# Kernel optimization log

Hardware: AMD Instinct MI355X
Metric: run time of the kernel (lower is better)

Reference implementation:

```python
import jax, jax.numpy as jnp
import numpy as np

N_CELLS = 50000
HID = 64
DEG = 16
K_NODES = 4  # nodes per cell; cell i owns nodes [4i, 4i+4)
SP = 3


def setup_inputs() -> dict:
    key = jax.random.key(0)
    ks = jax.random.split(key, 12)
    s = 1.0 / np.sqrt(HID)
    inp = {
        'features': jax.random.normal(ks[0], (N_CELLS, HID), jnp.float32),
        'positions': jax.random.normal(ks[1], (K_NODES * N_CELLS, SP), jnp.float32),
        'neighbors': jax.random.randint(ks[2], (N_CELLS, DEG), 0, N_CELLS, jnp.int32),
        # message MLP: Linear(2H+1 -> H), SiLU, Linear(H -> H)
        'W1': jax.random.normal(ks[3], (2 * HID + 1, HID), jnp.float32) * s,
        'b1': jnp.zeros((HID,), jnp.float32),
        'W2': jax.random.normal(ks[4], (HID, HID), jnp.float32) * s,
        'b2': jnp.zeros((HID,), jnp.float32),
        # update MLP: Linear(H + H -> H), SiLU, Linear(H -> H)
        'Wu1': jax.random.normal(ks[5], (2 * HID, HID), jnp.float32) * s,
        'bu1': jnp.zeros((HID,), jnp.float32),
        'Wu2': jax.random.normal(ks[6], (HID, HID), jnp.float32) * s,
        'bu2': jnp.zeros((HID,), jnp.float32),
    }
    return inp


def reference(features, positions, neighbors, W1, b1, W2, b2, Wu1, bu1, Wu2, bu2):
    N, H = features.shape
    # centroid of each cell's owned nodes (cell i -> nodes [K*i, K*i+K))
    cent = positions.reshape(N, K_NODES, SP).mean(axis=1)          # [N, sp]
    fj = features[neighbors]                                       # [N, D, H]
    cj = cent[neighbors]                                           # [N, D, sp]
    # centroid-distance geometric invariant per (cell, neighbor) pair
    geom = jnp.linalg.norm(cent[:, None, :] - cj, axis=-1, keepdims=True)  # [N, D, 1]
    fi = jnp.broadcast_to(features[:, None, :], fj.shape)          # [N, D, H]
    x = jnp.concatenate([fi, fj, geom], axis=-1)                   # [N, D, 2H+1]
    h = jax.nn.silu(x @ W1 + b1) @ W2 + b2                         # [N, D, H]
    msg = h.mean(axis=1)                                           # mean over neighbors
    u = jnp.concatenate([features, msg], axis=-1)                  # [N, 2H]
    upd = jax.nn.silu(u @ Wu1 + bu1) @ Wu2 + bu2
    updated_features = features + upd
    return updated_features, positions
```

## Files before the change

kernel.cpp:

```cpp
#include <hip/hip_runtime.h>


#define DEG 16

typedef __attribute__((ext_vector_type(8))) short short8;
typedef __attribute__((ext_vector_type(4))) float f32x4;
typedef uint2 uint2_a __attribute__((may_alias));
typedef uint4 uint4_a __attribute__((may_alias));
typedef unsigned short ushort_a __attribute__((may_alias));

union HbRd { uint4_a u; short8 s; };
union Frag { short8 s; uint4 u; };

__device__ __forceinline__ unsigned f2bf(float f) {
  unsigned u = __float_as_uint(f);
  return (u + 0x7FFFu + ((u >> 16) & 1u)) >> 16;
}
__device__ __forceinline__ float bf2f(unsigned bits16) {
  return __uint_as_float(bits16 << 16);
}
__device__ __forceinline__ float silu(float h) {
  return h / (1.f + __expf(-h));
}
__device__ __forceinline__ float silu_fast(float h) {
  return h * __builtin_amdgcn_rcpf(1.f + __expf(-h));
}

__global__ __launch_bounds__(256) void aux_kernel(
    const float* __restrict__ pos,
    const float* __restrict__ W1, const float* __restrict__ W2,
    const float* __restrict__ Wu1, const float* __restrict__ Wu2,
    float* __restrict__ outpos, float* __restrict__ cent4,
    unsigned short* __restrict__ w1pq, unsigned short* __restrict__ w2t,
    unsigned short* __restrict__ wu1t, unsigned short* __restrict__ wu2b)
{
  int t = blockIdx.x * 256 + threadIdx.x;
  if (t < 150000) {
    ((float4*)outpos)[t] = ((const float4*)pos)[t];
  } else if (t < 174576) {
    const int r = t - 150000;
    if (r < 8192) {
      const int j = r & 7, l = (r >> 3) & 15, q = (r >> 7) & 3;
      const int f = r >> 9, kk = f & 1, mt = f >> 1;
      const int k = kk * 32 + q * 8 + j;
      const int m = mt * 16 + l;
      w1pq[r] = (unsigned short)f2bf(
          (m < 64) ? W1[k * 64 + m] : W1[(k + 64) * 64 + (m - 64)]);
    } else if (r < 12288) {
      const int s = r - 8192;
      const int j = s & 7, l = (s >> 3) & 15, q = (s >> 7) & 3;
      const int f = s >> 9, kk = f & 1, mt = f >> 1;
      const int k = kk * 32 + q * 8 + j;
      w2t[s] = (unsigned short)f2bf(W2[k * 64 + mt * 16 + l]);
    } else if (r < 20480) {
      const int s = r - 12288;
      const int j = s & 7, l = (s >> 3) & 15, q = (s >> 7) & 3;
      const int f = s >> 9, kk = f & 3, mt = f >> 2;
      const int k = kk * 32 + q * 8 + j;
      wu1t[s] = (unsigned short)f2bf(Wu1[k * 64 + mt * 16 + l]);
    } else {
      const int s = r - 20480;
      const int j = s & 7, l = (s >> 3) & 15, q = (s >> 7) & 3;
      const int f = s >> 9, kk = f & 1, nt = f >> 1;
      const int k = kk * 32 + q * 8 + j;
      wu2b[s] = (unsigned short)f2bf(Wu2[k * 64 + nt * 16 + l]);
    }
  } else if (t < 224576) {
    const int i = t - 174576;
    const float4* pp = (const float4*)(pos + 12 * i);
    const float4 a = pp[0], b = pp[1], c = pp[2];
    float4 o;
    o.x = (a.x + a.w + b.z + c.y) * 0.25f;
    o.y = (a.y + b.x + b.w + c.z) * 0.25f;
    o.z = (a.z + b.y + c.x + c.w) * 0.25f;
    o.w = 0.f;
    ((float4*)cent4)[i] = o;
  }
}

__global__ __launch_bounds__(256) void prep_kernel(
    const float* __restrict__ feat,
    const unsigned short* __restrict__ w1pq,
    unsigned short* __restrict__ featb,
    unsigned char* __restrict__ Q8)
{
  const int lane = threadIdx.x & 63;
  const int wid  = threadIdx.x >> 6;
  const int quad = lane >> 4;
  const int l15  = lane & 15;
  const int tile = blockIdx.x * 4 + wid;
  const bool act = (tile < 3125);
  const int  tt  = act ? tile : 3124;
  const int  cr  = tt * 16 + l15;

  short8 xf[2];
  #pragma unroll
  for (int kk = 0; kk < 2; ++kk) {
    const float4 f0 = *(const float4*)(feat + cr * 64 + kk * 32 + quad * 8);
    const float4 f1 = *(const float4*)(feat + cr * 64 + kk * 32 + quad * 8 + 4);
    Frag v;
    v.s[0] = (short)f2bf(f0.x); v.s[1] = (short)f2bf(f0.y);
    v.s[2] = (short)f2bf(f0.z); v.s[3] = (short)f2bf(f0.w);
    v.s[4] = (short)f2bf(f1.x); v.s[5] = (short)f2bf(f1.y);
    v.s[6] = (short)f2bf(f1.z); v.s[7] = (short)f2bf(f1.w);
    xf[kk] = v.s;
    if (act) *(uint4*)(featb + cr * 64 + kk * 32 + quad * 8) = v.u;
  }

  short8 wf[4][2];
  #pragma unroll
  for (int m = 0; m < 4; ++m)
    #pragma unroll
    for (int kk = 0; kk < 2; ++kk)
      wf[m][kk] = *(const short8*)(w1pq + ((((m + 4) * 2 + kk) * 4 + quad) << 7) + l15 * 8);

  f32x4 acc[4] = {};
  #pragma unroll
  for (int kk = 0; kk < 2; ++kk)
    #pragma unroll
    for (int m = 0; m < 4; ++m)
      acc[m] = __builtin_amdgcn_mfma_f32_16x16x32_bf16(wf[m][kk], xf[kk], acc[m], 0, 0, 0);

  if (act) {
    #pragma unroll
    for (int m = 0; m < 4; ++m) {
      int w = __builtin_amdgcn_cvt_pk_fp8_f32(acc[m][0], acc[m][1], 0, false);
      w = __builtin_amdgcn_cvt_pk_fp8_f32(acc[m][2], acc[m][3], w, true);
      *(unsigned int*)(Q8 + cr * 64 + m * 16 + quad * 4) = (unsigned)w;
    }
  }
}

__global__ __launch_bounds__(256) void msg_tail_kernel(
    const unsigned short* __restrict__ featb,
    const unsigned char* __restrict__ Q8,
    const float4* __restrict__ cent4,
    const int* __restrict__ nbr,
    const float* __restrict__ feat,
    const unsigned short* __restrict__ w1pq,
    const unsigned short* __restrict__ w2t,
    const unsigned short* __restrict__ wu1t,
    const unsigned short* __restrict__ wu2b,
    const float* __restrict__ b1, const float* __restrict__ W1,
    const float* __restrict__ b2, const float* __restrict__ bu1,
    const float* __restrict__ bu2,
    float* __restrict__ outf)
{
  __shared__ uint4 smem[432];
  char* sT  = (char*)smem;
  char* Msg = sT + 2304;
  char* Hb  = sT + 4608;

  const int lane = threadIdx.x & 63;
  const int wid  = threadIdx.x >> 6;
  const int quad = lane >> 4;
  const int l15  = lane & 15;
  const int tile = blockIdx.x;
  const int cr   = tile * 16 + l15;

  {
    short8 wpf[2];
    #pragma unroll
    for (int kk = 0; kk < 2; ++kk)
      wpf[kk] = *(const short8*)(w1pq + (((wid * 2 + kk) * 4 + quad) << 7) + l15 * 8);
    f32x4 accp = {};
    #pragma unroll
    for (int kk = 0; kk < 2; ++kk) {
      const short8 bf = *(const short8*)(featb + cr * 64 + kk * 32 + quad * 8);
      accp = __builtin_amdgcn_mfma_f32_16x16x32_bf16(wpf[kk], bf, accp, 0, 0, 0);
    }
    uint2 pk;
    pk.x = f2bf(accp[0]) | (f2bf(accp[1]) << 16);
    pk.y = f2bf(accp[2]) | (f2bf(accp[3]) << 16);
    *(uint2_a*)(sT + l15 * 144 + wid * 32 + quad * 8) = pk;
  }

  __syncthreads();

  const float b1l = b1[lane];
  const float wl  = W1[8192 + lane];

  #pragma unroll
  for (int i = 0; i < 4; ++i) {
    const int c  = tile * 16 + wid * 4 + i;
    const int cs = __builtin_amdgcn_readfirstlane(c);
    const int* nrow = nbr + cs * DEG;

    const int njl = nrow[lane & 15];
    const float4 ci = cent4[cs];
    const float4 cj = cent4[njl];
    const float dx = ci.x - cj.x, dy = ci.y - cj.y, dz = ci.z - cj.z;
    const float g = sqrtf(dx * dx + dy * dy + dz * dz);

    const float pcb =
        bf2f(((const ushort_a*)(sT + (wid * 4 + i) * 144))[lane]) + b1l;

    float acc = 0.f;
    #pragma unroll
    for (int d = 0; d < DEG; ++d) {
      const int   nd = nrow[d];
      const float gd = __uint_as_float(
          __builtin_amdgcn_readlane((int)__float_as_uint(g), d));
      const float qv = __builtin_amdgcn_cvt_f32_fp8((int)Q8[nd * 64 + lane], 0);
      acc += silu_fast(pcb + qv + gd * wl);
    }
    ((ushort_a*)(sT + (wid * 4 + i) * 144))[lane] =
        (unsigned short)f2bf(acc * 0.0625f);
  }

  short8 w2f[2], wu1f[4], wu2f[2];
  #pragma unroll
  for (int kk = 0; kk < 2; ++kk)
    w2f[kk]  = *(const short8*)(w2t  + (((wid * 2 + kk) * 4 + quad) << 7) + l15 * 8);
  #pragma unroll
  for (int kk = 0; kk < 4; ++kk)
    wu1f[kk] = *(const short8*)(wu1t + (((wid * 4 + kk) * 4 + quad) << 7) + l15 * 8);
  #pragma unroll
  for (int kk = 0; kk < 2; ++kk)
    wu2f[kk] = *(const short8*)(wu2b + (((wid * 2 + kk) * 4 + quad) << 7) + l15 * 8);

  const f32x4 b2f  = *(const f32x4*)(b2  + wid * 16 + quad * 4);
  const f32x4 bu1f = *(const f32x4*)(bu1 + wid * 16 + quad * 4);
  const float bu2v = bu2[wid * 16 + l15];

  __syncthreads();

  f32x4 accm = {};
  #pragma unroll
  for (int kk = 0; kk < 2; ++kk) {
    HbRd t; t.u = *(const uint4_a*)(sT + l15 * 144 + kk * 64 + quad * 16);
    accm = __builtin_amdgcn_mfma_f32_16x16x32_bf16(w2f[kk], t.s, accm, 0, 0, 0);
  }
  {
    uint2 pk;
    pk.x = f2bf(accm[0] + b2f[0]) | (f2bf(accm[1] + b2f[1]) << 16);
    pk.y = f2bf(accm[2] + b2f[2]) | (f2bf(accm[3] + b2f[3]) << 16);
    *(uint2_a*)(Msg + l15 * 144 + wid * 32 + quad * 8) = pk;
  }
  __syncthreads();

  f32x4 accu = {};
  #pragma unroll
  for (int kk = 0; kk < 4; ++kk) {
    short8 bf;
    if (kk < 2) {
      bf = *(const short8*)(featb + cr * 64 + kk * 32 + quad * 8);
    } else {
      HbRd t; t.u = *(const uint4_a*)(Msg + l15 * 144 + (kk - 2) * 64 + quad * 16);
      bf = t.s;
    }
    accu = __builtin_amdgcn_mfma_f32_16x16x32_bf16(wu1f[kk], bf, accu, 0, 0, 0);
  }
  {
    float sv[4];
    #pragma unroll
    for (int rg = 0; rg < 4; ++rg)
      sv[rg] = silu(accu[rg] + bu1f[rg]);
    uint2 pk;
    pk.x = f2bf(sv[0]) | (f2bf(sv[1]) << 16);
    pk.y = f2bf(sv[2]) | (f2bf(sv[3]) << 16);
    *(uint2_a*)(Hb + l15 * 144 + wid * 32 + quad * 8) = pk;
  }
  __syncthreads();

  f32x4 acc2 = {};
  #pragma unroll
  for (int kk = 0; kk < 2; ++kk) {
    HbRd t; t.u = *(const uint4_a*)(Hb + l15 * 144 + kk * 64 + quad * 16);
    acc2 = __builtin_amdgcn_mfma_f32_16x16x32_bf16(t.s, wu2f[kk], acc2, 0, 0, 0);
  }
  #pragma unroll
  for (int rg = 0; rg < 4; ++rg) {
    const int row = tile * 16 + quad * 4 + rg;
    const int col = wid * 16 + l15;
    outf[row * 64 + col] = feat[row * 64 + col] + acc2[rg] + bu2v;
  }
}

extern "C" void kernel_launch(void* const* d_in, const int* in_sizes, int n_in,
                              void* d_out, int out_size, void* d_ws, size_t ws_size,
                              hipStream_t stream)
{
  const float* feat = (const float*)d_in[0];
  const float* pos  = (const float*)d_in[1];
  const int*   nbr  = (const int*)d_in[2];
  const float* W1   = (const float*)d_in[3];
  const float* b1   = (const float*)d_in[4];
  const float* W2   = (const float*)d_in[5];
  const float* b2   = (const float*)d_in[6];
  const float* Wu1  = (const float*)d_in[7];
  const float* bu1  = (const float*)d_in[8];
  const float* Wu2  = (const float*)d_in[9];
  const float* bu2  = (const float*)d_in[10];
  float* out = (float*)d_out;

  unsigned short* featb = (unsigned short*)d_ws;
  unsigned char*  Q8    = (unsigned char*)((char*)d_ws + 12800000);
  float*          cent4 = (float*)((char*)d_ws + 25600000);
  unsigned short* w1pq  = (unsigned short*)((char*)d_ws + 26400000);
  unsigned short* w2t   = (unsigned short*)((char*)d_ws + 26416384);
  unsigned short* wu1t  = (unsigned short*)((char*)d_ws + 26424576);
  unsigned short* wu2b  = (unsigned short*)((char*)d_ws + 26440960);

  aux_kernel<<<878, 256, 0, stream>>>(pos, W1, W2, Wu1, Wu2, out + 3200000,
                                      cent4, w1pq, w2t, wu1t, wu2b);
  prep_kernel<<<782, 256, 0, stream>>>(feat, w1pq, featb, Q8);
  msg_tail_kernel<<<3125, 256, 0, stream>>>(featb, Q8, (const float4*)cent4,
                                            nbr, feat, w1pq, w2t, wu1t, wu2b,
                                            b1, W1, b2, bu1, bu2, out);
}
```

Baseline: 120.4 us.

## Move position copy and centroid work into prep kernel; hoist geometry loads

Result: no change. 122.8 us (+2.0%).

```diff
diff --git a/kernel.cpp b/kernel.cpp
--- a/kernel.cpp
+++ b/kernel.cpp
@@ -26,69 +26,74 @@
   return h * __builtin_amdgcn_rcpf(1.f + __expf(-h));
 }
 
-__global__ __launch_bounds__(256) void aux_kernel(
-    const float* __restrict__ pos,
+__global__ __launch_bounds__(256) void wswz_kernel(
     const float* __restrict__ W1, const float* __restrict__ W2,
     const float* __restrict__ Wu1, const float* __restrict__ Wu2,
-    float* __restrict__ outpos, float* __restrict__ cent4,
     unsigned short* __restrict__ w1pq, unsigned short* __restrict__ w2t,
     unsigned short* __restrict__ wu1t, unsigned short* __restrict__ wu2b)
 {
-  int t = blockIdx.x * 256 + threadIdx.x;
-  if (t < 150000) {
-    ((float4*)outpos)[t] = ((const float4*)pos)[t];
-  } else if (t < 174576) {
-    const int r = t - 150000;
-    if (r < 8192) {
-      const int j = r & 7, l = (r >> 3) & 15, q = (r >> 7) & 3;
-      const int f = r >> 9, kk = f & 1, mt = f >> 1;
-      const int k = kk * 32 + q * 8 + j;
-      const int m = mt * 16 + l;
-      w1pq[r] = (unsigned short)f2bf(
-          (m < 64) ? W1[k * 64 + m] : W1[(k + 64) * 64 + (m - 64)]);
-    } else if (r < 12288) {
-      const int s = r - 8192;
-      const int j = s & 7, l = (s >> 3) & 15, q = (s >> 7) & 3;
-      const int f = s >> 9, kk = f & 1, mt = f >> 1;
-      const int k = kk * 32 + q * 8 + j;
-      w2t[s] = (unsigned short)f2bf(W2[k * 64 + mt * 16 + l]);
-    } else if (r < 20480) {
-      const int s = r - 12288;
-      const int j = s & 7, l = (s >> 3) & 15, q = (s >> 7) & 3;
-      const int f = s >> 9, kk = f & 3, mt = f >> 2;
-      const int k = kk * 32 + q * 8 + j;
-      wu1t[s] = (unsigned short)f2bf(Wu1[k * 64 + mt * 16 + l]);
-    } else {
-      const int s = r - 20480;
-      const int j = s & 7, l = (s >> 3) & 15, q = (s >> 7) & 3;
-      const int f = s >> 9, kk = f & 1, nt = f >> 1;
-      const int k = kk * 32 + q * 8 + j;
-      wu2b[s] = (unsigned short)f2bf(Wu2[k * 64 + nt * 16 + l]);
-    }
-  } else if (t < 224576) {
-    const int i = t - 174576;
-    const float4* pp = (const float4*)(pos + 12 * i);
-    const float4 a = pp[0], b = pp[1], c = pp[2];
-    float4 o;
-    o.x = (a.x + a.w + b.z + c.y) * 0.25f;
-    o.y = (a.y + b.x + b.w + c.z) * 0.25f;
-    o.z = (a.z + b.y + c.x + c.w) * 0.25f;
-    o.w = 0.f;
-    ((float4*)cent4)[i] = o;
+  const int r = blockIdx.x * 256 + threadIdx.x;
+  if (r < 8192) {
+    const int j = r & 7, l = (r >> 3) & 15, q = (r >> 7) & 3;
+    const int f = r >> 9, kk = f & 1, mt = f >> 1;
+    const int k = kk * 32 + q * 8 + j;
+    const int m = mt * 16 + l;
+    w1pq[r] = (unsigned short)f2bf(
+        (m < 64) ? W1[k * 64 + m] : W1[(k + 64) * 64 + (m - 64)]);
+  } else if (r < 12288) {
+    const int s = r - 8192;
+    const int j = s & 7, l = (s >> 3) & 15, q = (s >> 7) & 3;
+    const int f = s >> 9, kk = f & 1, mt = f >> 1;
+    const int k = kk * 32 + q * 8 + j;
+    w2t[s] = (unsigned short)f2bf(W2[k * 64 + mt * 16 + l]);
+  } else if (r < 20480) {
+    const int s = r - 12288;
+    const int j = s & 7, l = (s >> 3) & 15, q = (s >> 7) & 3;
+    const int f = s >> 9, kk = f & 3, mt = f >> 2;
+    const int k = kk * 32 + q * 8 + j;
+    wu1t[s] = (unsigned short)f2bf(Wu1[k * 64 + mt * 16 + l]);
+  } else if (r < 24576) {
+    const int s = r - 20480;
+    const int j = s & 7, l = (s >> 3) & 15, q = (s >> 7) & 3;
+    const int f = s >> 9, kk = f & 1, nt = f >> 1;
+    const int k = kk * 32 + q * 8 + j;
+    wu2b[s] = (unsigned short)f2bf(Wu2[k * 64 + nt * 16 + l]);
   }
 }
 
 __global__ __launch_bounds__(256) void prep_kernel(
-    const float* __restrict__ feat,
+    const float* __restrict__ feat, const float* __restrict__ pos,
     const unsigned short* __restrict__ w1pq,
     unsigned short* __restrict__ featb,
-    unsigned char* __restrict__ Q8)
+    unsigned char* __restrict__ Q8,
+    float* __restrict__ outpos, float* __restrict__ cent4)
 {
+  const int b = blockIdx.x;
+  if (b >= 1368) {
+    const int i = (b - 1368) * 256 + threadIdx.x;
+    if (i < 50000) {
+      const float4* pp = (const float4*)(pos + 12 * i);
+      const float4 a = pp[0], bb = pp[1], c = pp[2];
+      float4 o;
+      o.x = (a.x + a.w + bb.z + c.y) * 0.25f;
+      o.y = (a.y + bb.x + bb.w + c.z) * 0.25f;
+      o.z = (a.z + bb.y + c.x + c.w) * 0.25f;
+      o.w = 0.f;
+      ((float4*)cent4)[i] = o;
+    }
+    return;
+  }
+  if (b >= 782) {
+    const int t = (b - 782) * 256 + threadIdx.x;
+    if (t < 150000) ((float4*)outpos)[t] = ((const float4*)pos)[t];
+    return;
+  }
+
   const int lane = threadIdx.x & 63;
   const int wid  = threadIdx.x >> 6;
   const int quad = lane >> 4;
   const int l15  = lane & 15;
-  const int tile = blockIdx.x * 4 + wid;
+  const int tile = b * 4 + wid;
   const bool act = (tile < 3125);
   const int  tt  = act ? tile : 3124;
   const int  cr  = tt * 16 + l15;
@@ -180,25 +185,29 @@
   const float b1l = b1[lane];
   const float wl  = W1[8192 + lane];
 
+  const int*  nrow[4];
+  float g4[4];
   #pragma unroll
   for (int i = 0; i < 4; ++i) {
-    const int c  = tile * 16 + wid * 4 + i;
-    const int cs = __builtin_amdgcn_readfirstlane(c);
-    const int* nrow = nbr + cs * DEG;
-
-    const int njl = nrow[lane & 15];
+    const int cs = __builtin_amdgcn_readfirstlane(tile * 16 + wid * 4 + i);
+    nrow[i] = nbr + cs * DEG;
+    const int njl = nrow[i][lane & 15];
     const float4 ci = cent4[cs];
     const float4 cj = cent4[njl];
     const float dx = ci.x - cj.x, dy = ci.y - cj.y, dz = ci.z - cj.z;
-    const float g = sqrtf(dx * dx + dy * dy + dz * dz);
-
+    g4[i] = sqrtf(dx * dx + dy * dy + dz * dz);
+  }
+
+  #pragma unroll
+  for (int i = 0; i < 4; ++i) {
     const float pcb =
         bf2f(((const ushort_a*)(sT + (wid * 4 + i) * 144))[lane]) + b1l;
+    const float g = g4[i];
 
     float acc = 0.f;
     #pragma unroll
     for (int d = 0; d < DEG; ++d) {
-      const int   nd = nrow[d];
+      const int   nd = nrow[i][d];
       const float gd = __uint_as_float(
           __builtin_amdgcn_readlane((int)__float_as_uint(g), d));
       const float qv = __builtin_amdgcn_cvt_f32_fp8((int)Q8[nd * 64 + lane], 0);
@@ -302,9 +311,10 @@
   unsigned short* wu1t  = (unsigned short*)((char*)d_ws + 26424576);
   unsigned short* wu2b  = (unsigned short*)((char*)d_ws + 26440960);
 
-  aux_kernel<<<878, 256, 0, stream>>>(pos, W1, W2, Wu1, Wu2, out + 3200000,
-                                      cent4, w1pq, w2t, wu1t, wu2b);
-  prep_kernel<<<782, 256, 0, stream>>>(feat, w1pq, featb, Q8);
+  wswz_kernel<<<96, 256, 0, stream>>>(W1, W2, Wu1, Wu2,
+                                      w1pq, w2t, wu1t, wu2b);
+  prep_kernel<<<1564, 256, 0, stream>>>(feat, pos, w1pq, featb, Q8,
+                                        out + 3200000, cent4);
   msg_tail_kernel<<<3125, 256, 0, stream>>>(featb, Q8, (const float4*)cent4,
                                             nbr, feat, w1pq, w2t, wu1t, wu2b,
                                             b1, W1, b2, bu1, bu2, out);
```
